# Kernel optimization log

Measured on AMD Instinct MI355X. Metric: run time of the kernel, lower is better.

## Reference

```python
import math
import jax, jax.numpy as jnp
import numpy as np

NEG = -1.0e10  # matches LARGE_NUMBER padding in the original
K_SUBSET = 8
N_SAMPLES = 2


def log_conv(aL, aR, K):
    """Log-space convolution of two count distributions, truncated to counts 0..K-1.
    aL, aR: [..., K] log-values; returns c[m] = logsumexp_j aL[j] + aR[m-j]."""
    jj = jnp.arange(K)[:, None]
    mm = jnp.arange(K)[None, :]
    idx = mm - jj  # [K(j), K(m)]
    valid = idx >= 0
    aRg = aR[..., jnp.clip(idx, 0, K - 1)]  # [..., K, K]
    t = aL[..., :, None] + jnp.where(valid, aRg, NEG)
    return jax.nn.logsumexp(t, axis=-2)


def up_pass(theta, k):
    """theta: [B, N] logits (N power of two). Returns list of per-level log-ESP
    tables, levels[l]: [B, N/2^l, k+1]; levels[-1][:,0,j] = log e_j(exp theta)."""
    B, N = theta.shape
    K = k + 1
    leaf = jnp.full((B, N, K), NEG, theta.dtype)
    leaf = leaf.at[..., 0].set(0.0).at[..., 1].set(theta)
    levels = [leaf]
    a = leaf
    while a.shape[1] > 1:
        a = log_conv(a[:, 0::2], a[:, 1::2], K)
        levels.append(a)
    return levels


def down_marginals(levels, theta, k):
    """Exact inclusion marginals P(x_i=1 | sum=k) via tree forward-backward."""
    K = k + 1
    B = theta.shape[0]
    ext = jnp.full((B, 1, K), NEG, theta.dtype).at[..., 0].set(0.0)
    for lvl in range(len(levels) - 2, -1, -1):
        a = levels[lvl]
        aL, aR = a[:, 0::2], a[:, 1::2]
        extL = log_conv(ext, aR, K)  # ESP of everything outside left subtree
        extR = log_conv(ext, aL, K)
        ext = jnp.stack([extL, extR], axis=2).reshape(B, a.shape[1], K)
    logZ = levels[-1][:, 0, k]  # log e_k over all items
    # P(x_i=1) = exp(theta_i) * e_{k-1}(others) / e_k(all)
    return jnp.exp(theta + ext[..., k - 1] - logZ[:, None])


def sample_counts(levels, k, n_samples, key):
    """Top-down exact sampling of k-subsets; returns leaf counts [S, B, N] in {0,1}."""
    K = k + 1
    B = levels[0].shape[0]
    counts = jnp.full((n_samples, B, 1), k, jnp.int32)
    jj = jnp.arange(K)
    for lvl in range(len(levels) - 2, -1, -1):
        a = levels[lvl]
        aL, aR = a[:, 0::2], a[:, 1::2]
        n = aL.shape[1]
        idx = counts[..., None] - jj  # desired right-count, [S,B,n,K]
        valid = idx >= 0
        aRg = jnp.take_along_axis(
            jnp.broadcast_to(aR[None], (n_samples, B, n, K)),
            jnp.clip(idx, 0, k), axis=-1)
        logits = aL[None] + jnp.where(valid, aRg, NEG)
        key, sub = jax.random.split(key)
        g = jax.random.gumbel(sub, logits.shape, logits.dtype)
        cL = jnp.argmax(logits + g, axis=-1).astype(jnp.int32)
        cR = counts - cL
        counts = jnp.stack([cL, cR], axis=-1).reshape(n_samples, B, 2 * n)
    return counts


def setup_inputs() -> dict:
    key = jax.random.key(0)
    scores = jax.random.normal(key, (8192, 32, 8), dtype=jnp.float32)
    return {"scores": scores}


def reference(scores):
    nnodes, choices, ensemble = scores.shape
    k = min(K_SUBSET, choices)
    flat = jnp.transpose(scores, (0, 2, 1)).reshape(nnodes * ensemble, choices)
    N = 2 ** math.ceil(math.log2(choices))
    if N > choices:
        flat = jnp.concatenate(
            [flat, jnp.full((flat.shape[0], N - choices), NEG, flat.dtype)], axis=1)
    levels = up_pass(flat, k)
    marg_flat = down_marginals(levels, flat, k)[:, :choices]  # [B, choices]
    marginals = jnp.transpose(
        marg_flat.reshape(nnodes, ensemble, choices), (0, 2, 1))  # [nnodes, choices, ensemble]
    counts = sample_counts(levels, k, N_SAMPLES, jax.random.key(42))
    counts = counts[:, :, :choices].astype(scores.dtype)
    samples = jnp.transpose(
        counts.reshape(N_SAMPLES, nnodes, ensemble, choices), (0, 1, 3, 2))
    # straight-through: hard samples forward, marginal gradients backward
    samples = jax.lax.stop_gradient(samples - marginals[None]) + marginals[None]
    return samples, marginals
```

## Files before the change

### kernel.cpp

```cpp
#include <hip/hip_runtime.h>
#include <stdint.h>


__host__ __device__ __forceinline__ void tf2x32(uint32_t k0, uint32_t k1,
                                                uint32_t x0, uint32_t x1,
                                                uint32_t& y0, uint32_t& y1) {
  const uint32_t ks[3] = {k0, k1, k0 ^ k1 ^ 0x1BD11BDAu};
  x0 += ks[0]; x1 += ks[1];
  const int R0[4] = {13, 15, 26, 6};
  const int R1[4] = {17, 29, 16, 24};
#pragma unroll
  for (int i = 0; i < 5; ++i) {
    const int* R = (i & 1) ? R1 : R0;
#pragma unroll
    for (int rr = 0; rr < 4; ++rr) {
      x0 += x1;
      x1 = (x1 << R[rr]) | (x1 >> (32 - R[rr]));
      x1 ^= x0;
    }
    x0 += ks[(i + 1) % 3];
    x1 += ks[(i + 2) % 3] + (uint32_t)(i + 1);
  }
  y0 = x0; y1 = x1;
}

struct TFKeys { uint32_t v[10]; };

__device__ __attribute__((noinline)) float gumbel_draw(uint32_t sk0,
                                                       uint32_t sk1,
                                                       uint32_t f) {
  uint32_t y0, y1;
  tf2x32(sk0, sk1, 0u, f, y0, y1);
  uint32_t bits = y0 ^ y1;
  uint32_t fb = (bits >> 9) | 0x3f800000u;
  float u = __uint_as_float(fb) - 1.0f;
  const float tiny = 1.17549435e-38f;
  float rr = fmaxf(tiny, u + tiny);
  return -logf(-logf(rr));
}

template<bool FAST> __device__ __forceinline__ float expT(float x) {
  return FAST ? __expf(x) : expf(x);
}
template<bool FAST> __device__ __forceinline__ float logT(float x) {
  return FAST ? __logf(x) : logf(x);
}

template<int SIN, int SOUT, bool FAST, bool LS>
__device__ __forceinline__ void conv_level(const float (&aL)[SIN],
                                           const float (&aR)[SIN],
                                           float (&o)[SOUT]) {
#pragma unroll
  for (int m = 1; m < SOUT; ++m) {
    if (LS && m == SOUT - 1) { o[m] = aL[SIN - 1] + aR[SIN - 1]; continue; }
    const int jlo = (m - (SIN - 1) > 0) ? (m - (SIN - 1)) : 0;
    const int jhi = (m < SIN - 1) ? m : (SIN - 1);
    float t[SIN];
#pragma unroll
    for (int j = 0; j < SIN; ++j)
      if (j >= jlo && j <= jhi) t[j] = aL[j] + aR[m - j];
    float amax = t[jlo];
#pragma unroll
    for (int j = 0; j < SIN; ++j)
      if (j > jlo && j <= jhi) amax = fmaxf(amax, t[j]);
    float s = 0.0f;
#pragma unroll
    for (int j = 0; j < SIN; ++j)
      if (j >= jlo && j <= jhi) s += expT<FAST>(t[j] - amax);
    o[m] = logT<FAST>(s) + amax;
  }
}

template<int SSIB, int MLO, int MHI, bool FAST>
__device__ __forceinline__ void ext_level(const float (&ein)[8],
                                          const float* sib, float (&eo)[8]) {
#pragma unroll
  for (int m = MLO; m <= MHI; ++m) {
    const int jlo = (m - (SSIB - 1) > 0) ? (m - (SSIB - 1)) : 0;
    float t[8];
#pragma unroll
    for (int j = 0; j < 8; ++j)
      if (j >= jlo && j <= m) t[j] = ein[j] + sib[m - j];
    float amax = t[jlo];
#pragma unroll
    for (int j = 0; j < 8; ++j)
      if (j > jlo && j <= m) amax = fmaxf(amax, t[j]);
    float s = 0.0f;
#pragma unroll
    for (int j = 0; j < 8; ++j)
      if (j >= jlo && j <= m) s += expT<FAST>(t[j] - amax);
    eo[m] = logT<FAST>(s) + amax;
  }
}

#define ENT 128

__global__ __launch_bounds__(64, 4) void simple_sampler_kernel(
    const float* __restrict__ scores, float* __restrict__ out,
    int nnodes, TFKeys keys) {
  const int lane = threadIdx.x;
  const int q = lane & 3;
  const int r = lane >> 2;
  const int p = q & 1;
  const int g = q >> 1;
  const int row = blockIdx.x * 16 + r;
  const int node = row >> 3, e = row & 7;
  const int B = nnodes * 8;

  __shared__ float tab[ENT * 17];
#define L(E) tab[(E) * 17 + r]

  float th[8];
  const float* sc = scores + node * 256 + e + (16 * p + 8 * g) * 8;
#pragma unroll
  for (int c = 0; c < 8; ++c) th[c] = sc[c * 8];
#pragma unroll
  for (int c = 0; c < 8; ++c) L(16 * p + 8 * g + c) = th[c];

  float l1r[4], th2r[4];
#pragma unroll
  for (int n1l = 0; n1l < 4; ++n1l) {
    float tL = th[2 * n1l], tR = th[2 * n1l + 1];
    float amax = fmaxf(tR, tL);
    float s = expf(fminf(tR, tL) - amax) + 1.0f;
    l1r[n1l] = logf(s) + amax;
    th2r[n1l] = tL + tR;
    int n1 = 8 * p + 4 * g + n1l;
    L(32 + n1) = l1r[n1l];
    L(48 + n1) = th2r[n1l];
  }
  float l2r[2][5];
#pragma unroll
  for (int n2l = 0; n2l < 2; ++n2l) {
    float aL[3] = {0.0f, l1r[2 * n2l], th2r[2 * n2l]};
    float aR[3] = {0.0f, l1r[2 * n2l + 1], th2r[2 * n2l + 1]};
    float o5[5];
    conv_level<3, 5, false, true>(aL, aR, o5);
    l2r[n2l][0] = 0.0f;
    int n2 = 4 * p + 2 * g + n2l;
#pragma unroll
    for (int m = 1; m < 5; ++m) { l2r[n2l][m] = o5[m]; L(64 + n2 * 4 + m - 1) = o5[m]; }
  }
  float l3r[9];
  {
    float o9[9];
    conv_level<5, 9, false, true>(l2r[0], l2r[1], o9);
    l3r[0] = 0.0f;
    int n3 = 2 * p + g;
#pragma unroll
    for (int m = 1; m < 9; ++m) { l3r[m] = o9[m]; L(96 + n3 * 8 + m - 1) = o9[m]; }
  }

  __builtin_amdgcn_wave_barrier();

  float l3s[9];
  l3s[0] = 0.0f;
#pragma unroll
  for (int m = 1; m < 9; ++m) l3s[m] = __shfl_xor(l3r[m], 2);

  float A0[9], A1[9];
  {
    float aLp[9], aRp[9];
#pragma unroll
    for (int m = 0; m < 9; ++m) {
      aLp[m] = g ? l3s[m] : l3r[m];
      aRp[m] = g ? l3r[m] : l3s[m];
    }
    float own[4];
#pragma unroll
    for (int mi = 0; mi < 4; ++mi) {
      float t[8];
#pragma unroll
      for (int j = 0; j <= 2 * mi + 1; ++j) {
        float aRv = g ? aRp[2 * mi + 2 - j] : aRp[2 * mi + 1 - j];
        t[j] = aLp[j] + aRv;
      }
      float tlast = aLp[2 * mi + 2] + aRp[0];
      float amax = t[0];
#pragma unroll
      for (int j = 1; j <= 2 * mi + 1; ++j) amax = fmaxf(amax, t[j]);
      amax = g ? fmaxf(amax, tlast) : amax;
      float s = 0.0f;
#pragma unroll
      for (int j = 0; j <= 2 * mi + 1; ++j) s += expf(t[j] - amax);
      s += g ? expf(tlast - amax) : 0.0f;
      own[mi] = logf(s) + amax;
    }
    float l4o[9];
#pragma unroll
    for (int mi = 0; mi < 4; ++mi) {
      float oth = __shfl_xor(own[mi], 2);
      l4o[2 * mi + 1] = g ? oth : own[mi];
      l4o[2 * mi + 2] = g ? own[mi] : oth;
    }
    A0[0] = 0.0f; A1[0] = 0.0f;
#pragma unroll
    for (int m = 1; m < 9; ++m) {
      float o = l4o[m];
      float oth2 = __shfl_xor(o, 1);
      A0[m] = p ? oth2 : o;
      A1[m] = p ? o : oth2;
    }
  }

  float logZ;
  {
    float tv[9];
#pragma unroll
    for (int j = 0; j < 9; ++j) tv[j] = A0[j] + A1[8 - j];
    float amax = tv[0];
#pragma unroll
    for (int j = 1; j < 9; ++j) amax = fmaxf(amax, tv[j]);
    float s = 0.0f;
#pragma unroll
    for (int j = 0; j < 9; ++j) s += __expf(tv[j] - amax);
    logZ = __logf(s) + amax;
  }

  {
    float e4v[8];
    e4v[0] = 0.0f;
#pragma unroll
    for (int m = 1; m < 8; ++m) e4v[m] = p ? A0[m] : A1[m];
    float* mb = out + 2 * B * 32 + node * 256 + e;
    float e3[8];
    ext_level<9, 0, 7, true>(e4v, l3s, e3);
#pragma unroll
    for (int c2 = 0; c2 < 2; ++c2) {
      float e2v[8];
      ext_level<5, 4, 7, true>(e3, l2r[c2 ^ 1], e2v);
#pragma unroll
      for (int c1i = 0; c1i < 2; ++c1i) {
        const int n1l = 2 * c2 + c1i;
        float sib1[3] = {0.0f, l1r[n1l ^ 1], th2r[n1l ^ 1]};
        float e1m[8];
        ext_level<3, 6, 7, true>(e2v, sib1, e1m);
        const int colL = 16 * p + 8 * g + 2 * n1l;
        {
          float t6 = e1m[6] + th[2 * n1l + 1];
          float t7 = e1m[7];
          float amax = fmaxf(t6, t7);
          float s = __expf(t6 - amax) + __expf(t7 - amax);
          mb[colL * 8] = __expf((th[2 * n1l] + (__logf(s) + amax)) - logZ);
        }
        {
          float t6 = e1m[6] + th[2 * n1l];
          float t7 = e1m[7];
          float amax = fmaxf(t6, t7);
          float s = __expf(t6 - amax) + __expf(t7 - amax);
          mb[(colL + 1) * 8] = __expf((th[2 * n1l + 1] + (__logf(s) + amax)) - logZ);
        }
      }
    }
  }

  const int smp = q & 1;
  const int h = q >> 1;
  const uint32_t t9 = (uint32_t)(smp * B + row) * 9u;
  int c;
  {
    float bv = 0.0f; int bj = 0;
#pragma unroll
    for (int k = 0; k < 5; ++k) {
      const int j = 4 * h + k;
      float gd = gumbel_draw(keys.v[0], keys.v[1], t9 + (uint32_t)j);
      float v = (A0[j] + A1[8 - j]) + gd;
      if (k == 0) { bv = v; bj = j; } else if (v > bv) { bv = v; bj = j; }
    }
    float ov = __shfl_xor(bv, 2);
    int   oj = __shfl_xor(bj, 2);
    float vlo = h ? ov : bv;  int jlo = h ? oj : bj;
    float vhi = h ? bv : ov;  int jhi = h ? bj : oj;
    int rootj = (vhi > vlo) ? jhi : jlo;
    c = h ? (8 - rootj) : rootj;
  }
  int cA, cB;
  {
    int j0 = 0;
    if (c > 0) {
      float b0 = -3.0e38f;
      for (int j = 0; j <= c; ++j) {
        float a = (j == 0) ? 0.0f : L(96 + 16 * h + j - 1);
        float b = (c - j == 0) ? 0.0f : L(96 + 16 * h + 8 + (c - j) - 1);
        float gd = gumbel_draw(keys.v[2], keys.v[3],
                               2u * t9 + (uint32_t)(9 * h + j));
        float v = (a + b) + gd;
        if (v > b0) { b0 = v; j0 = j; }
      }
    }
    cA = j0; cB = c - j0;
  }
  uint32_t pk2 = 0;
  {
    int cc0 = cA, cc1 = cB;
#pragma unroll
    for (int i2 = 0; i2 < 2; ++i2) {
      const int i = 2 * h + i2;
      int ci = i2 ? cc1 : cc0;
      float best = -3.0e38f; int bj2 = 0;
#pragma unroll
      for (int j = 0; j < 5; ++j) {
        float gd = gumbel_draw(keys.v[4], keys.v[5],
                               4u * t9 + (uint32_t)(i * 9 + j));
        int idx = ci - j;
        int cl = min(max(idx, 1), 4);
        float b = L(64 + (2 * i + 1) * 4 + cl - 1);
        float bf = (idx == 0) ? 0.0f : b;
        float a = (j == 0) ? 0.0f : L(64 + (2 * i) * 4 + j - 1);
        float v = (a + bf) + gd;
        if (idx >= 0 && idx <= 4 && v > best) { best = v; bj2 = j; }
      }
      pk2 |= ((uint32_t)bj2 << (8 * i2)) | ((uint32_t)(ci - bj2) << (8 * i2 + 4));
    }
  }
  uint32_t pk3 = 0;
  {
    const uint32_t sk0 = keys.v[6], sk1 = keys.v[7];
    const uint32_t fb0 = 8u * t9;
#pragma unroll 2
    for (int i2 = 0; i2 < 4; ++i2) {
      const int i = 4 * h + i2;
      int ci = (int)((pk2 >> (4 * i2)) & 15u);
      float aL1 = L(32 + 2 * i), aL2 = L(48 + 2 * i);
      float bR1 = L(32 + 2 * i + 1), bR2 = L(48 + 2 * i + 1);
      uint32_t fb = fb0 + (uint32_t)(i * 9);
      float best = -3.0e38f; int bj3 = 0;
#pragma unroll
      for (int j = 0; j < 3; ++j) {
        float gd = gumbel_draw(sk0, sk1, fb + (uint32_t)j);
        int idx = ci - j;
        float bf = (idx == 1) ? bR1 : ((idx == 2) ? bR2 : 0.0f);
        float af = (j == 0) ? 0.0f : ((j == 1) ? aL1 : aL2);
        float v = (af + bf) + gd;
        if (idx >= 0 && idx <= 2 && v > best) { best = v; bj3 = j; }
      }
      pk3 |= ((uint32_t)bj3 << (8 * i2)) | ((uint32_t)(ci - bj3) << (8 * i2 + 4));
    }
  }
  {
    const uint32_t sk0 = keys.v[8], sk1 = keys.v[9];
    const uint32_t fb0 = 16u * t9;
    float* bs = out + smp * (B * 32) + node * 256 + e;
    uint32_t lst = 0; int m4 = 0;
#pragma unroll
    for (int i2 = 0; i2 < 8; ++i2) {
      int ci = (int)((pk3 >> (4 * i2)) & 15u);
      const int i = 8 * h + i2;
      if (ci == 1) {
        lst |= ((uint32_t)i2) << (4 * m4);
        ++m4;
      } else {
        int bj = ci >> 1;
        bs[16 * i] = (float)bj;
        bs[16 * i + 8] = (float)(ci - bj);
      }
    }
    for (int tt = 0; tt < m4; ++tt) {
      int i2 = (int)((lst >> (4 * tt)) & 15u);
      int i = 8 * h + i2;
      float thL = L(2 * i);
      float thR = L(2 * i + 1);
      uint32_t fb = fb0 + (uint32_t)(i * 9);
      float g0 = gumbel_draw(sk0, sk1, fb);
      float g1 = gumbel_draw(sk0, sk1, fb + 1u);
      int bj = ((thL + g1) > (thR + g0)) ? 1 : 0;
      bs[16 * i] = (float)bj;
      bs[16 * i + 8] = (float)(1 - bj);
    }
  }
#undef L
}

extern "C" void kernel_launch(void* const* d_in, const int* in_sizes, int n_in,
                              void* d_out, int out_size, void* d_ws, size_t ws_size,
                              hipStream_t stream) {
  const float* scores = (const float*)d_in[0];
  float* out = (float*)d_out;
  const int nnodes = in_sizes[0] / (32 * 8);
  const int B = nnodes * 8;

  TFKeys K;
  uint32_t k0 = 0u, k1 = 42u;
  for (int t = 0; t < 5; ++t) {
    uint32_t n0, n1, s0, s1;
    tf2x32(k0, k1, 0u, 0u, n0, n1);
    tf2x32(k0, k1, 0u, 1u, s0, s1);
    K.v[2 * t] = s0; K.v[2 * t + 1] = s1;
    k0 = n0; k1 = n1;
  }

  dim3 grid((unsigned)(B / 16)), block(64);
  hipLaunchKernelGGL(simple_sampler_kernel, grid, block, 0, stream,
                     scores, out, nnodes, K);
}
```

Before: 121.9 us.

## Balance top-down sampling work across lane pairs and inline gumbel draws

The level-1 and level-2 sampling loops now split the valid (subtree, split) candidates evenly between the two lanes of a pair, instead of each lane handling its own subtree with variable trip counts. Each lane keeps running argmaxes, and partners merge them with shuffles that break ties by lower index. Level-2 loops now visit only valid j values rather than all five. gumbel_draw is force-inlined instead of noinline, which removes call overhead but may raise register pressure.

```diff
diff --git a/kernel.cpp b/kernel.cpp
--- a/kernel.cpp
+++ b/kernel.cpp
@@ -26,9 +26,8 @@
 
 struct TFKeys { uint32_t v[10]; };
 
-__device__ __attribute__((noinline)) float gumbel_draw(uint32_t sk0,
-                                                       uint32_t sk1,
-                                                       uint32_t f) {
+__device__ __forceinline__ float gumbel_draw(uint32_t sk0, uint32_t sk1,
+                                             uint32_t f) {
   uint32_t y0, y1;
   tf2x32(sk0, sk1, 0u, f, y0, y1);
   uint32_t bits = y0 ^ y1;
@@ -257,7 +256,7 @@
   const int smp = q & 1;
   const int h = q >> 1;
   const uint32_t t9 = (uint32_t)(smp * B + row) * 9u;
-  int c;
+  int rootj;
   {
     float bv = 0.0f; int bj = 0;
 #pragma unroll
@@ -271,47 +270,84 @@
     int   oj = __shfl_xor(bj, 2);
     float vlo = h ? ov : bv;  int jlo = h ? oj : bj;
     float vhi = h ? bv : ov;  int jhi = h ? bj : oj;
-    int rootj = (vhi > vlo) ? jhi : jlo;
-    c = h ? (8 - rootj) : rootj;
+    rootj = (vhi > vlo) ? jhi : jlo;
   }
   int cA, cB;
   {
-    int j0 = 0;
-    if (c > 0) {
-      float b0 = -3.0e38f;
-      for (int j = 0; j <= c; ++j) {
-        float a = (j == 0) ? 0.0f : L(96 + 16 * h + j - 1);
-        float b = (c - j == 0) ? 0.0f : L(96 + 16 * h + 8 + (c - j) - 1);
-        float gd = gumbel_draw(keys.v[2], keys.v[3],
-                               2u * t9 + (uint32_t)(9 * h + j));
-        float v = (a + b) + gd;
-        if (v > b0) { b0 = v; j0 = j; }
-      }
-    }
-    cA = j0; cB = c - j0;
+    const int c0r = rootj, c1r = 8 - rootj;
+    const int n0 = c0r ? c0r + 1 : 0;
+    const int n1c = c1r ? c1r + 1 : 0;
+    const int tot = n0 + n1c;
+    float b0 = -3.0e38f, b1 = -3.0e38f;
+    int j0 = 0, j1 = 0;
+    for (int t = h; t < tot; t += 2) {
+      const bool is1 = (t >= n0);
+      const int j = is1 ? (t - n0) : t;
+      const int ii = is1 ? 1 : 0;
+      const int cc = is1 ? c1r : c0r;
+      const int idx = cc - j;
+      float a = (j == 0) ? 0.0f : L(96 + 16 * ii + j - 1);
+      float b = (idx == 0) ? 0.0f : L(96 + 16 * ii + 8 + idx - 1);
+      float gd = gumbel_draw(keys.v[2], keys.v[3],
+                             2u * t9 + (uint32_t)(9 * ii + j));
+      float v = (a + b) + gd;
+      if (is1) { if (v > b1) { b1 = v; j1 = j; } }
+      else     { if (v > b0) { b0 = v; j0 = j; } }
+    }
+    {
+      float ob0 = __shfl_xor(b0, 2); int oj0 = __shfl_xor(j0, 2);
+      float ob1 = __shfl_xor(b1, 2); int oj1 = __shfl_xor(j1, 2);
+      if (!(b0 > ob0 || (b0 == ob0 && j0 <= oj0))) j0 = oj0;
+      if (!(b1 > ob1 || (b1 == ob1 && j1 <= oj1))) j1 = oj1;
+    }
+    const int jh = h ? j1 : j0;
+    const int ch = h ? c1r : c0r;
+    cA = jh; cB = ch - jh;
   }
   uint32_t pk2 = 0;
   {
-    int cc0 = cA, cc1 = cB;
-#pragma unroll
-    for (int i2 = 0; i2 < 2; ++i2) {
-      const int i = 2 * h + i2;
-      int ci = i2 ? cc1 : cc0;
-      float best = -3.0e38f; int bj2 = 0;
-#pragma unroll
-      for (int j = 0; j < 5; ++j) {
-        float gd = gumbel_draw(keys.v[4], keys.v[5],
-                               4u * t9 + (uint32_t)(i * 9 + j));
-        int idx = ci - j;
-        int cl = min(max(idx, 1), 4);
-        float b = L(64 + (2 * i + 1) * 4 + cl - 1);
-        float bf = (idx == 0) ? 0.0f : b;
-        float a = (j == 0) ? 0.0f : L(64 + (2 * i) * 4 + j - 1);
-        float v = (a + bf) + gd;
-        if (idx >= 0 && idx <= 4 && v > best) { best = v; bj2 = j; }
-      }
-      pk2 |= ((uint32_t)bj2 << (8 * i2)) | ((uint32_t)(ci - bj2) << (8 * i2 + 4));
-    }
+    const int oA = __shfl_xor(cA, 2), oB = __shfl_xor(cB, 2);
+    const int tc0 = h ? oA : cA, tc1 = h ? oB : cB;
+    const int tc2 = h ? cA : oA, tc3 = h ? cB : oB;
+    const int jl0 = max(0, tc0 - 4), nf0 = min(4, tc0) - jl0 + 1;
+    const int jl1 = max(0, tc1 - 4), nf1 = min(4, tc1) - jl1 + 1;
+    const int jl2 = max(0, tc2 - 4), nf2 = min(4, tc2) - jl2 + 1;
+    const int jl3 = max(0, tc3 - 4), nf3 = min(4, tc3) - jl3 + 1;
+    const int s1 = nf0, s2 = s1 + nf1, s3 = s2 + nf2, tot = s3 + nf3;
+    float bv0 = -3.0e38f, bv1 = -3.0e38f, bv2 = -3.0e38f, bv3 = -3.0e38f;
+    int bj0 = 0, bj1 = 0, bj2 = 0, bj3 = 0;
+    for (int t = h; t < tot; t += 2) {
+      const int i = (t >= s1) + (t >= s2) + (t >= s3);
+      const int base = (i == 0) ? 0 : ((i == 1) ? s1 : ((i == 2) ? s2 : s3));
+      const int jlo = (i == 0) ? jl0 : ((i == 1) ? jl1 : ((i == 2) ? jl2 : jl3));
+      const int ci  = (i == 0) ? tc0 : ((i == 1) ? tc1 : ((i == 2) ? tc2 : tc3));
+      const int j = jlo + (t - base);
+      const int idx = ci - j;
+      float a = (j == 0) ? 0.0f : L(64 + (2 * i) * 4 + j - 1);
+      float b = (idx == 0) ? 0.0f : L(64 + (2 * i + 1) * 4 + idx - 1);
+      float gd = gumbel_draw(keys.v[4], keys.v[5],
+                             4u * t9 + (uint32_t)(i * 9 + j));
+      float v = (a + b) + gd;
+      if (i == 0)      { if (v > bv0) { bv0 = v; bj0 = j; } }
+      else if (i == 1) { if (v > bv1) { bv1 = v; bj1 = j; } }
+      else if (i == 2) { if (v > bv2) { bv2 = v; bj2 = j; } }
+      else             { if (v > bv3) { bv3 = v; bj3 = j; } }
+    }
+    {
+      float ob; int oj;
+      ob = __shfl_xor(bv0, 2); oj = __shfl_xor(bj0, 2);
+      if (!(bv0 > ob || (bv0 == ob && bj0 <= oj))) bj0 = oj;
+      ob = __shfl_xor(bv1, 2); oj = __shfl_xor(bj1, 2);
+      if (!(bv1 > ob || (bv1 == ob && bj1 <= oj))) bj1 = oj;
+      ob = __shfl_xor(bv2, 2); oj = __shfl_xor(bj2, 2);
+      if (!(bv2 > ob || (bv2 == ob && bj2 <= oj))) bj2 = oj;
+      ob = __shfl_xor(bv3, 2); oj = __shfl_xor(bj3, 2);
+      if (!(bv3 > ob || (bv3 == ob && bj3 <= oj))) bj3 = oj;
+    }
+    const int jA = h ? bj2 : bj0;  const int cTA = h ? tc2 : tc0;
+    const int jB = h ? bj3 : bj1;  const int cTB = h ? tc3 : tc1;
+    pk2 = (uint32_t)jA | ((uint32_t)(cTA - jA) << 4)
+        | ((uint32_t)jB << 8) | ((uint32_t)(cTB - jB) << 12);
   }
   uint32_t pk3 = 0;
   {
```

New measurement: 119.7 us. About the same (-1.9%).
